# Optimization experiments

Hardware: AMD Instinct MI355X
Metric: run time of the kernel (lower is better)

## Reference

```python
import jax, jax.numpy as jnp
import numpy as np

B, S, D = 2, 2048, 1024
H, DK, DV = 16, 64, 64
D_OUT = 1024


def setup_inputs() -> dict:
    key = jax.random.key(0)
    ks = jax.random.split(key, 9)
    sd = 1.0 / np.sqrt(D)
    # Linear weights stored as [in, out] (torch applies x @ W.T with W [out,in])
    return {
        "x": jax.random.normal(ks[0], (B, S, D), dtype=jnp.float32),
        "Wq": jax.random.normal(ks[1], (D, H * DK), dtype=jnp.float32) * sd,
        "bq": jnp.zeros((H * DK,), dtype=jnp.float32),
        "Wk": jax.random.normal(ks[2], (D, H * DK), dtype=jnp.float32) * sd,
        "bk": jnp.zeros((H * DK,), dtype=jnp.float32),
        "Wv": jax.random.normal(ks[3], (D, H * DV), dtype=jnp.float32) * sd,
        "bv": jnp.zeros((H * DV,), dtype=jnp.float32),
        "Wo": jax.random.normal(ks[4], (H * DV, D_OUT), dtype=jnp.float32) * sd,
        "bo": jnp.zeros((D_OUT,), dtype=jnp.float32),
    }


def _attn(x, Wq, bq, Wk, bk, Wv, bv, Wo, bo):
    n = x.shape[-2]
    q = (x @ Wq + bq).reshape(B, n, H, DK).transpose(0, 2, 1, 3)  # [B,H,S,DK]
    k = (x @ Wk + bk).reshape(B, n, H, DK).transpose(0, 2, 1, 3)
    v = (x @ Wv + bv).reshape(B, n, H, DV).transpose(0, 2, 1, 3)
    scores = jnp.einsum("bhqd,bhkd->bhqk", q / jnp.sqrt(jnp.float32(DK)), k)
    # causal additive mask: 0 on/below diagonal, -inf above (matches 1 - 1/tril)
    causal = jnp.tril(jnp.ones((n, n), dtype=bool))
    scores = jnp.where(causal, scores, -jnp.inf)
    probs = jax.nn.softmax(scores, axis=-1)
    out = jnp.einsum("bhqk,bhkd->bhqd", probs, v)  # [B,H,S,DV]
    out = out.transpose(0, 2, 1, 3).reshape(B, n, H * DV)
    return out @ Wo + bo


def reference(x, Wq, bq, Wk, bk, Wv, bv, Wo, bo):
    return _attn(x, Wq, bq, Wk, bk, Wv, bv, Wo, bo)
```

## Files before the change

### kernel.cpp

```cpp
#include <hip/hip_runtime.h>

typedef unsigned short u16;
typedef __bf16 bf16_t;
typedef bf16_t bf16x8 __attribute__((ext_vector_type(8)));
typedef float f32x4 __attribute__((ext_vector_type(4)));

#define DEV __device__ __forceinline__
#define LOG2E 1.4426950408889634f
#define QKS (0.125f * LOG2E)

static_assert(sizeof(bf16x8) == 16, "bf16x8 must be 16B");

DEV u16 f2b(float v) { return __builtin_bit_cast(u16, (bf16_t)v); }
DEV float b2f(u16 v) { return (float)__builtin_bit_cast(bf16_t, v); }

DEV void g2l16(const void* g, void* l) {
  __builtin_amdgcn_global_load_lds(
      (const __attribute__((address_space(1))) void*)g,
      (__attribute__((address_space(3))) void*)l, 16, 0, 0);
}

DEV int sniff_is_f32(const u16* __restrict__ W) {
  const int lane = threadIdx.x & 63;
  int cnt = 0;
#pragma unroll
  for (int i = 0; i < 8; i++) {
    u16 u = W[(lane * 8 + i) * 2];
    cnt += (((u >> 7) & 0xFF) >= 126) ? 1 : 0;
  }
#pragma unroll
  for (int off = 1; off < 64; off <<= 1) cnt += __shfl_xor(cnt, off, 64);
  return cnt > 128;
}


__global__ __launch_bounds__(256) void convert_x_k(
    const void* __restrict__ xin, const u16* __restrict__ Wsniff,
    u16* __restrict__ xb) {
  const int i = (blockIdx.x * 256 + threadIdx.x) * 8;
  if (sniff_is_f32(Wsniff)) {
    const float* xf = (const float*)xin;
    float4 a = *(const float4*)&xf[i];
    float4 b = *(const float4*)&xf[i + 4];
    u16 o[8] = {f2b(a.x), f2b(a.y), f2b(a.z), f2b(a.w),
                f2b(b.x), f2b(b.y), f2b(b.z), f2b(b.w)};
    *(uint4*)&xb[i] = *(const uint4*)o;
  } else {
    *(uint4*)&xb[i] = *(const uint4*)((const u16*)xin + i);
  }
}

__global__ __launch_bounds__(256) void transpose_k(
    const void* __restrict__ Wq, const void* __restrict__ Wk,
    const void* __restrict__ Wv, const void* __restrict__ Wo,
    const void* __restrict__ bq, const void* __restrict__ bk,
    const void* __restrict__ bv, const void* __restrict__ bo,
    u16* __restrict__ Wqkv_t, u16* __restrict__ Wo_t,
    u16* __restrict__ bqkv_b, u16* __restrict__ bo_b) {
  __shared__ u16 tile[64][68];
  const int z = blockIdx.z;
  const void* src = (z == 0) ? Wq : (z == 1) ? Wk : (z == 2) ? Wv : Wo;
  u16* dst = (z < 3) ? (Wqkv_t + (size_t)z * 1024 * 1024) : Wo_t;
  const int k0 = blockIdx.y * 64, n0 = blockIdx.x * 64;
  const int t = threadIdx.x;
  const int r = t >> 4, c4 = (t & 15) * 4;
  const int isf = sniff_is_f32((const u16*)Wq);

  if (blockIdx.x == 0 && blockIdx.y == 0) {
    const void* bsrc = (z == 0) ? bq : (z == 1) ? bk : (z == 2) ? bv : bo;
    u16* bdst = (z < 3) ? (bqkv_b + z * 1024) : bo_b;
#pragma unroll
    for (int i = 0; i < 4; i++) {
      const int idx = t + i * 256;
      const float v =
          isf ? ((const float*)bsrc)[idx] : b2f(((const u16*)bsrc)[idx]);
      bdst[idx] = f2b(v);
    }
  }

#pragma unroll
  for (int i = 0; i < 4; i++) {
    int rr = r + i * 16;
    const size_t base = (size_t)(k0 + rr) * 1024 + n0 + c4;
    if (isf) {
      float4 v = *(const float4*)((const float*)src + base);
      tile[rr][c4] = f2b(v.x); tile[rr][c4 + 1] = f2b(v.y);
      tile[rr][c4 + 2] = f2b(v.z); tile[rr][c4 + 3] = f2b(v.w);
    } else {
      ushort4 v = *(const ushort4*)((const u16*)src + base);
      tile[rr][c4] = v.x; tile[rr][c4 + 1] = v.y;
      tile[rr][c4 + 2] = v.z; tile[rr][c4 + 3] = v.w;
    }
  }
  __syncthreads();
#pragma unroll
  for (int i = 0; i < 4; i++) {
    int rr = r + i * 16;
    ushort4 v;
    v.x = tile[c4][rr]; v.y = tile[c4 + 1][rr];
    v.z = tile[c4 + 2][rr]; v.w = tile[c4 + 3][rr];
    *(ushort4*)&dst[(size_t)(n0 + rr) * 1024 + k0 + c4] = v;
  }
}

template <int MODE>
__global__ __launch_bounds__(256, 3) void gemm_k(
    const u16* __restrict__ A, const u16* __restrict__ Bt,
    const u16* __restrict__ bias, void* __restrict__ o0v,
    u16* __restrict__ o1, u16* __restrict__ o2,
    const u16* __restrict__ Wsniff, int M, int N, int K) {
  alignas(16) __shared__ u16 As[128][32];
  alignas(16) __shared__ u16 Bs[128][32];
  const int tid = threadIdx.x;
  const int wave = tid >> 6, lane = tid & 63;
  const int quad = lane >> 4, l16 = lane & 15;
  const int m0 = blockIdx.y * 128, n0 = blockIdx.x * 128;
  const int wr = (wave >> 1) * 64, wc = (wave & 1) * 64;

  f32x4 acc[4][4];
#pragma unroll
  for (int i = 0; i < 4; i++)
#pragma unroll
    for (int j = 0; j < 4; j++) acc[i][j] = (f32x4){0.f, 0.f, 0.f, 0.f};

  const int srow = lane >> 2, scol = (lane & 3) * 8;
  for (int k0 = 0; k0 < K; k0 += 32) {
    __syncthreads();
#pragma unroll
    for (int j = 0; j < 4; j++) {
      const int t = wave * 4 + j;
      if (t < 8) {
        const int row = t * 16 + srow;
        g2l16(&A[(size_t)(m0 + row) * K + k0 + scol], &As[t * 16][0]);
      } else {
        const int rb = t - 8;
        const int row = rb * 16 + srow;
        g2l16(&Bt[(size_t)(n0 + row) * K + k0 + scol], &Bs[rb * 16][0]);
      }
    }
    __syncthreads();
    bf16x8 af[4], bfr[4];
#pragma unroll
    for (int mi = 0; mi < 4; mi++)
      af[mi] = *(const bf16x8*)&As[wr + mi * 16 + l16][quad * 8];
#pragma unroll
    for (int ni = 0; ni < 4; ni++)
      bfr[ni] = *(const bf16x8*)&Bs[wc + ni * 16 + l16][quad * 8];
#pragma unroll
    for (int mi = 0; mi < 4; mi++)
#pragma unroll
      for (int ni = 0; ni < 4; ni++)
        acc[mi][ni] = __builtin_amdgcn_mfma_f32_16x16x32_bf16(
            af[mi], bfr[ni], acc[mi][ni], 0, 0, 0);
  }

  const int isf = (MODE == 1) ? sniff_is_f32(Wsniff) : 0;
#pragma unroll
  for (int mi = 0; mi < 4; mi++) {
    const int rbase = m0 + wr + mi * 16 + quad * 4;
#pragma unroll
    for (int ni = 0; ni < 4; ni++) {
      const int col = n0 + wc + ni * 16 + l16;
      const float bv_ = b2f(bias[col]);
      if (MODE == 0) {
        const int seg = col >> 10;
        const int nn = col & 1023;
        const int h = nn >> 6, d = nn & 63;
        u16* op = (seg == 0) ? (u16*)o0v : (seg == 1) ? o1 : o2;
#pragma unroll
        for (int r = 0; r < 4; r++) {
          const int m = rbase + r;
          const int b = m >> 11, s = m & 2047;
          float v = acc[mi][ni][r] + bv_;
          if (seg == 0) v *= QKS;
          if (seg < 2)
            op[(((size_t)(b * 16 + h) * 2048) + s) * 64 + d] = f2b(v);
          else
            op[(((size_t)(b * 16 + h) * 64) + d) * 2048 + s] = f2b(v);
        }
      } else {
#pragma unroll
        for (int r = 0; r < 4; r++) {
          const int m = rbase + r;
          const float v = acc[mi][ni][r] + bv_;
          if (isf) ((float*)o0v)[(size_t)m * N + col] = v;
          else     ((u16*)o0v)[(size_t)m * N + col] = f2b(v);
        }
      }
    }
  }
}

__global__ __launch_bounds__(256, 3) void attn_k(
    const u16* __restrict__ Q, const u16* __restrict__ K,
    const u16* __restrict__ Vt, u16* __restrict__ O) {
  alignas(16) __shared__ u16 Ks[2][2][64][32];
  alignas(16) __shared__ u16 Vs[2][2][64][32];
  alignas(16) __shared__ u16 Ps[128][72];
  const int tid = threadIdx.x;
  const int wave = tid >> 6, lane = tid & 63;
  const int quad = lane >> 4, l16 = lane & 15;
  const int qt = 15 - (int)blockIdx.x;
  const int bh = blockIdx.y;
  const int b = bh >> 4, h = bh & 15;
  const int q0 = qt * 128;
  const int wrow = q0 + wave * 32;

  bf16x8 aq[2][2];
#pragma unroll
  for (int mi = 0; mi < 2; mi++)
#pragma unroll
    for (int kc = 0; kc < 2; kc++)
      aq[mi][kc] = *(const bf16x8*)&Q[((size_t)bh * 2048 + wrow + mi * 16 + l16) *
                                          64 + kc * 32 + quad * 8];

  f32x4 oacc[2][4];
#pragma unroll
  for (int mi = 0; mi < 2; mi++)
#pragma unroll
    for (int di = 0; di < 4; di++) oacc[mi][di] = (f32x4){0.f, 0.f, 0.f, 0.f};
  float lrow[2][4] = {{0.f, 0.f, 0.f, 0.f}, {0.f, 0.f, 0.f, 0.f}};

  const int srow = lane >> 2, scol = (lane & 3) * 8;
  auto stage = [&](int buf, int kts) {
    const int k0s = kts * 64;
#pragma unroll
    for (int j = 0; j < 4; j++) {
      const int t = wave * 4 + j;
      if (t < 8) {
        const int kc = t >> 2, rb = t & 3;
        g2l16(&K[((size_t)bh * 2048 + k0s + rb * 16 + srow) * 64 + kc * 32 + scol],
              &Ks[buf][kc][rb * 16][0]);
      } else {
        const int tt = t - 8;
        const int kc = tt >> 2, rb = tt & 3;
        g2l16(&Vt[((size_t)bh * 64 + rb * 16 + srow) * 2048 + k0s + kc * 32 + scol],
              &Vs[buf][kc][rb * 16][0]);
      }
    }
  };

  const int nkt = 2 * qt + 2;
  stage(0, 0);
  for (int kt = 0; kt < nkt; kt++) {
    const int cur = kt & 1;
    const int k0 = kt * 64;
    if (kt + 1 < nkt) {
      stage(cur ^ 1, kt + 1);
      asm volatile("s_waitcnt vmcnt(4)" ::: "memory");
    } else {
      asm volatile("s_waitcnt vmcnt(0)" ::: "memory");
    }
    asm volatile("s_barrier" ::: "memory");

    const bool skip = (k0 > wrow + 31);
    if (!skip) {
      const bool needmask = (k0 + 63 > wrow);
      f32x4 sacc[2][4];
#pragma unroll
      for (int mi = 0; mi < 2; mi++)
#pragma unroll
        for (int ni = 0; ni < 4; ni++) sacc[mi][ni] = (f32x4){0.f, 0.f, 0.f, 0.f};
#pragma unroll
      for (int kc = 0; kc < 2; kc++)
#pragma unroll
        for (int ni = 0; ni < 4; ni++) {
          bf16x8 bk_ = *(const bf16x8*)&Ks[cur][kc][ni * 16 + l16][quad * 8];
#pragma unroll
          for (int mi = 0; mi < 2; mi++)
            sacc[mi][ni] = __builtin_amdgcn_mfma_f32_16x16x32_bf16(
                aq[mi][kc], bk_, sacc[mi][ni], 0, 0, 0);
        }

#pragma unroll
      for (int mi = 0; mi < 2; mi++) {
        const int rowb = wrow + mi * 16 + quad * 4;
#pragma unroll
        for (int ni = 0; ni < 4; ni++) {
          const int col = k0 + ni * 16 + l16;
#pragma unroll
          for (int r = 0; r < 4; r++) {
            float p = __builtin_amdgcn_exp2f(sacc[mi][ni][r]);
            if (needmask && (col > rowb + r)) p = 0.f;
            lrow[mi][r] += p;
            Ps[wave * 32 + mi * 16 + quad * 4 + r][ni * 16 + l16] = f2b(p);
          }
        }
      }
      asm volatile("s_waitcnt lgkmcnt(0)" ::: "memory");

#pragma unroll
      for (int kc = 0; kc < 2; kc++) {
        bf16x8 ap[2];
#pragma unroll
        for (int mi = 0; mi < 2; mi++)
          ap[mi] = *(const bf16x8*)&Ps[wave * 32 + mi * 16 + l16][kc * 32 + quad * 8];
#pragma unroll
        for (int di = 0; di < 4; di++) {
          bf16x8 bv_ = *(const bf16x8*)&Vs[cur][kc][di * 16 + l16][quad * 8];
#pragma unroll
          for (int mi = 0; mi < 2; mi++)
            oacc[mi][di] = __builtin_amdgcn_mfma_f32_16x16x32_bf16(
                ap[mi], bv_, oacc[mi][di], 0, 0, 0);
        }
      }
    }
    asm volatile("s_barrier" ::: "memory");
  }

#pragma unroll
  for (int mi = 0; mi < 2; mi++)
#pragma unroll
    for (int r = 0; r < 4; r++) {
#pragma unroll
      for (int off = 1; off < 16; off <<= 1)
        lrow[mi][r] += __shfl_xor(lrow[mi][r], off, 64);
    }

#pragma unroll
  for (int mi = 0; mi < 2; mi++)
#pragma unroll
    for (int di = 0; di < 4; di++)
#pragma unroll
      for (int r = 0; r < 4; r++) {
        const int row = q0 + wave * 32 + mi * 16 + quad * 4 + r;
        const float v = oacc[mi][di][r] / lrow[mi][r];
        O[((size_t)b * 2048 + row) * 1024 + h * 64 + di * 16 + l16] = f2b(v);
      }
}

extern "C" void kernel_launch(void* const* d_in, const int* in_sizes, int n_in,
                              void* d_out, int out_size, void* d_ws,
                              size_t ws_size, hipStream_t stream) {
  const void* x  = d_in[0];
  const void* Wq = d_in[1];
  const void* bq = d_in[2];
  const void* Wk = d_in[3];
  const void* bk = d_in[4];
  const void* Wv = d_in[5];
  const void* bv = d_in[6];
  const void* Wo = d_in[7];
  const void* bo = d_in[8];

  char* ws = (char*)d_ws;
  u16* xb     = (u16*)ws;          ws += (size_t)4096 * 1024 * 2;
  u16* Wqkv_t = (u16*)ws;          ws += (size_t)3072 * 1024 * 2;
  u16* Wo_t   = (u16*)ws;          ws += (size_t)1024 * 1024 * 2;
  u16* bqkv_b = (u16*)ws;          ws += 3072 * 2;
  u16* bo_b   = (u16*)ws;          ws += 1024 * 2 + 128;
  u16* Qb     = (u16*)ws;          ws += (size_t)4096 * 1024 * 2;
  u16* Kb     = (u16*)ws;          ws += (size_t)4096 * 1024 * 2;
  u16* Vtb    = (u16*)ws;          ws += (size_t)4096 * 1024 * 2;
  u16* Ob     = xb;

  convert_x_k<<<2048, 256, 0, stream>>>(x, (const u16*)Wq, xb);
  transpose_k<<<dim3(16, 16, 4), 256, 0, stream>>>(Wq, Wk, Wv, Wo, bq, bk, bv,
                                                   bo, Wqkv_t, Wo_t, bqkv_b,
                                                   bo_b);
  gemm_k<0><<<dim3(24, 32), 256, 0, stream>>>(xb, Wqkv_t, bqkv_b, Qb, Kb, Vtb,
                                              (const u16*)Wq, 4096, 3072, 1024);
  attn_k<<<dim3(16, 32), 256, 0, stream>>>(Qb, Kb, Vtb, Ob);
  gemm_k<1><<<dim3(8, 32), 256, 0, stream>>>(Ob, Wo_t, bo_b, d_out, nullptr,
                                             nullptr, (const u16*)Wq, 4096,
                                             1024, 1024);
}
```

Baseline: 236.7 us.

## Pair causal query tiles per block and stage 128-key swizzled K/V tiles

```diff
diff --git a/kernel.cpp b/kernel.cpp
--- a/kernel.cpp
+++ b/kernel.cpp
@@ -191,142 +191,157 @@
   }
 }
 
-__global__ __launch_bounds__(256, 3) void attn_k(
+__global__ __launch_bounds__(256, 1) void attn_k(
     const u16* __restrict__ Q, const u16* __restrict__ K,
     const u16* __restrict__ Vt, u16* __restrict__ O) {
-  alignas(16) __shared__ u16 Ks[2][2][64][32];
-  alignas(16) __shared__ u16 Vs[2][2][64][32];
+  alignas(16) __shared__ u16 Ks[2][128][64];
+  alignas(16) __shared__ u16 Vs[2][64][128];
   alignas(16) __shared__ u16 Ps[128][72];
   const int tid = threadIdx.x;
   const int wave = tid >> 6, lane = tid & 63;
   const int quad = lane >> 4, l16 = lane & 15;
-  const int qt = 15 - (int)blockIdx.x;
   const int bh = blockIdx.y;
   const int b = bh >> 4, h = bh & 15;
-  const int q0 = qt * 128;
-  const int wrow = q0 + wave * 32;
-
-  bf16x8 aq[2][2];
-#pragma unroll
-  for (int mi = 0; mi < 2; mi++)
-#pragma unroll
-    for (int kc = 0; kc < 2; kc++)
-      aq[mi][kc] = *(const bf16x8*)&Q[((size_t)bh * 2048 + wrow + mi * 16 + l16) *
-                                          64 + kc * 32 + quad * 8];
-
-  f32x4 oacc[2][4];
-#pragma unroll
-  for (int mi = 0; mi < 2; mi++)
-#pragma unroll
-    for (int di = 0; di < 4; di++) oacc[mi][di] = (f32x4){0.f, 0.f, 0.f, 0.f};
-  float lrow[2][4] = {{0.f, 0.f, 0.f, 0.f}, {0.f, 0.f, 0.f, 0.f}};
-
-  const int srow = lane >> 2, scol = (lane & 3) * 8;
-  auto stage = [&](int buf, int kts) {
-    const int k0s = kts * 64;
-#pragma unroll
-    for (int j = 0; j < 4; j++) {
-      const int t = wave * 4 + j;
-      if (t < 8) {
-        const int kc = t >> 2, rb = t & 3;
-        g2l16(&K[((size_t)bh * 2048 + k0s + rb * 16 + srow) * 64 + kc * 32 + scol],
-              &Ks[buf][kc][rb * 16][0]);
+  const int sw = l16 & 7;
+
+  const int krow_off = lane >> 3, kchunk = lane & 7;
+  const int vrow_off = lane >> 4, vchunk = lane & 15;
+
+  for (int pi = 0; pi < 2; pi++) {
+    const int qt = pi ? (15 - (int)blockIdx.x) : (int)blockIdx.x;
+    const int q0 = qt * 128;
+    const int wrow = q0 + wave * 32;
+    const int nkt = qt + 1;
+
+    bf16x8 aq[2][2];
+#pragma unroll
+    for (int mi = 0; mi < 2; mi++)
+#pragma unroll
+      for (int kcD = 0; kcD < 2; kcD++)
+        aq[mi][kcD] = *(const bf16x8*)&Q[((size_t)bh * 2048 + wrow + mi * 16 +
+                                          l16) * 64 + kcD * 32 + quad * 8];
+
+    f32x4 oacc[2][4];
+#pragma unroll
+    for (int mi = 0; mi < 2; mi++)
+#pragma unroll
+      for (int di = 0; di < 4; di++) oacc[mi][di] = (f32x4){0.f, 0.f, 0.f, 0.f};
+    float lrow[2][4] = {{0.f, 0.f, 0.f, 0.f}, {0.f, 0.f, 0.f, 0.f}};
+
+    auto stage = [&](int buf, int kts) {
+      const int k0s = kts * 128;
+#pragma unroll
+      for (int j = 0; j < 8; j++) {
+        const int t = wave * 8 + j;
+        if (t < 16) {
+          const int r = t * 8 + krow_off;
+          const int cs = kchunk ^ (r & 7);
+          g2l16(&K[((size_t)bh * 2048 + k0s + r) * 64 + cs * 8],
+                &Ks[buf][t * 8][0]);
+        } else {
+          const int t2 = t - 16;
+          const int r = t2 * 4 + vrow_off;
+          const int cs = vchunk ^ (r & 7);
+          g2l16(&Vt[((size_t)bh * 64 + r) * 2048 + k0s + cs * 8],
+                &Vs[buf][t2 * 4][0]);
+        }
+      }
+    };
+
+    stage(0, 0);
+    for (int kt = 0; kt < nkt; kt++) {
+      const int cur = kt & 1;
+      const int k0 = kt * 128;
+      if (kt + 1 < nkt) {
+        stage(cur ^ 1, kt + 1);
+        asm volatile("s_waitcnt vmcnt(8)" ::: "memory");
       } else {
-        const int tt = t - 8;
-        const int kc = tt >> 2, rb = tt & 3;
-        g2l16(&Vt[((size_t)bh * 64 + rb * 16 + srow) * 2048 + k0s + kc * 32 + scol],
-              &Vs[buf][kc][rb * 16][0]);
-      }
-    }
-  };
-
-  const int nkt = 2 * qt + 2;
-  stage(0, 0);
-  for (int kt = 0; kt < nkt; kt++) {
-    const int cur = kt & 1;
-    const int k0 = kt * 64;
-    if (kt + 1 < nkt) {
-      stage(cur ^ 1, kt + 1);
-      asm volatile("s_waitcnt vmcnt(4)" ::: "memory");
-    } else {
-      asm volatile("s_waitcnt vmcnt(0)" ::: "memory");
-    }
-    asm volatile("s_barrier" ::: "memory");
-
-    const bool skip = (k0 > wrow + 31);
-    if (!skip) {
-      const bool needmask = (k0 + 63 > wrow);
-      f32x4 sacc[2][4];
-#pragma unroll
-      for (int mi = 0; mi < 2; mi++)
-#pragma unroll
-        for (int ni = 0; ni < 4; ni++) sacc[mi][ni] = (f32x4){0.f, 0.f, 0.f, 0.f};
-#pragma unroll
-      for (int kc = 0; kc < 2; kc++)
-#pragma unroll
-        for (int ni = 0; ni < 4; ni++) {
-          bf16x8 bk_ = *(const bf16x8*)&Ks[cur][kc][ni * 16 + l16][quad * 8];
+        asm volatile("s_waitcnt vmcnt(0)" ::: "memory");
+      }
+      asm volatile("s_barrier" ::: "memory");
+
+      for (int h2 = 0; h2 < 2; h2++) {
+        const int k0h = k0 + h2 * 64;
+        if (k0h > wrow + 31) continue;
+        const bool needmask = (k0h + 63 > wrow);
+
+        f32x4 sacc[2][4];
+#pragma unroll
+        for (int mi = 0; mi < 2; mi++)
+#pragma unroll
+          for (int ni = 0; ni < 4; ni++)
+            sacc[mi][ni] = (f32x4){0.f, 0.f, 0.f, 0.f};
+#pragma unroll
+        for (int kcD = 0; kcD < 2; kcD++)
+#pragma unroll
+          for (int ni = 0; ni < 4; ni++) {
+            const int pos = ((kcD << 2) | quad) ^ sw;
+            bf16x8 bk_ =
+                *(const bf16x8*)&Ks[cur][h2 * 64 + ni * 16 + l16][pos * 8];
+#pragma unroll
+            for (int mi = 0; mi < 2; mi++)
+              sacc[mi][ni] = __builtin_amdgcn_mfma_f32_16x16x32_bf16(
+                  aq[mi][kcD], bk_, sacc[mi][ni], 0, 0, 0);
+          }
+
+#pragma unroll
+        for (int mi = 0; mi < 2; mi++) {
+          const int rowb = wrow + mi * 16 + quad * 4;
+#pragma unroll
+          for (int ni = 0; ni < 4; ni++) {
+            const int col = k0h + ni * 16 + l16;
+#pragma unroll
+            for (int r = 0; r < 4; r++) {
+              float p = __builtin_amdgcn_exp2f(sacc[mi][ni][r]);
+              if (needmask && (col > rowb + r)) p = 0.f;
+              lrow[mi][r] += p;
+              Ps[wave * 32 + mi * 16 + quad * 4 + r][ni * 16 + l16] = f2b(p);
+            }
+          }
+        }
+        asm volatile("s_waitcnt lgkmcnt(0)" ::: "memory");
+
+#pragma unroll
+        for (int kc = 0; kc < 2; kc++) {
+          bf16x8 ap[2];
 #pragma unroll
           for (int mi = 0; mi < 2; mi++)
-            sacc[mi][ni] = __builtin_amdgcn_mfma_f32_16x16x32_bf16(
-                aq[mi][kc], bk_, sacc[mi][ni], 0, 0, 0);
-        }
-
-#pragma unroll
-      for (int mi = 0; mi < 2; mi++) {
-        const int rowb = wrow + mi * 16 + quad * 4;
-#pragma unroll
-        for (int ni = 0; ni < 4; ni++) {
-          const int col = k0 + ni * 16 + l16;
-#pragma unroll
-          for (int r = 0; r < 4; r++) {
-            float p = __builtin_amdgcn_exp2f(sacc[mi][ni][r]);
-            if (needmask && (col > rowb + r)) p = 0.f;
-            lrow[mi][r] += p;
-            Ps[wave * 32 + mi * 16 + quad * 4 + r][ni * 16 + l16] = f2b(p);
+            ap[mi] = *(const bf16x8*)&Ps[wave * 32 + mi * 16 + l16]
+                                        [kc * 32 + quad * 8];
+#pragma unroll
+          for (int di = 0; di < 4; di++) {
+            const int pos = ((h2 << 3) | (kc << 2) | quad) ^ sw;
+            bf16x8 bv_ = *(const bf16x8*)&Vs[cur][di * 16 + l16][pos * 8];
+#pragma unroll
+            for (int mi = 0; mi < 2; mi++)
+              oacc[mi][di] = __builtin_amdgcn_mfma_f32_16x16x32_bf16(
+                  ap[mi], bv_, oacc[mi][di], 0, 0, 0);
           }
         }
       }
-      asm volatile("s_waitcnt lgkmcnt(0)" ::: "memory");
-
-#pragma unroll
-      for (int kc = 0; kc < 2; kc++) {
-        bf16x8 ap[2];
-#pragma unroll
-        for (int mi = 0; mi < 2; mi++)
-          ap[mi] = *(const bf16x8*)&Ps[wave * 32 + mi * 16 + l16][kc * 32 + quad * 8];
-#pragma unroll
-        for (int di = 0; di < 4; di++) {
-          bf16x8 bv_ = *(const bf16x8*)&Vs[cur][kc][di * 16 + l16][quad * 8];
-#pragma unroll
-          for (int mi = 0; mi < 2; mi++)
-            oacc[mi][di] = __builtin_amdgcn_mfma_f32_16x16x32_bf16(
-                ap[mi], bv_, oacc[mi][di], 0, 0, 0);
-        }
-      }
-    }
-    asm volatile("s_barrier" ::: "memory");
-  }
-
-#pragma unroll
-  for (int mi = 0; mi < 2; mi++)
-#pragma unroll
-    for (int r = 0; r < 4; r++) {
-#pragma unroll
-      for (int off = 1; off < 16; off <<= 1)
-        lrow[mi][r] += __shfl_xor(lrow[mi][r], off, 64);
-    }
-
-#pragma unroll
-  for (int mi = 0; mi < 2; mi++)
-#pragma unroll
-    for (int di = 0; di < 4; di++)
+      asm volatile("s_barrier" ::: "memory");
+    }
+
+#pragma unroll
+    for (int mi = 0; mi < 2; mi++)
 #pragma unroll
       for (int r = 0; r < 4; r++) {
-        const int row = q0 + wave * 32 + mi * 16 + quad * 4 + r;
-        const float v = oacc[mi][di][r] / lrow[mi][r];
-        O[((size_t)b * 2048 + row) * 1024 + h * 64 + di * 16 + l16] = f2b(v);
-      }
+#pragma unroll
+        for (int off = 1; off < 16; off <<= 1)
+          lrow[mi][r] += __shfl_xor(lrow[mi][r], off, 64);
+      }
+
+#pragma unroll
+    for (int mi = 0; mi < 2; mi++)
+#pragma unroll
+      for (int di = 0; di < 4; di++)
+#pragma unroll
+        for (int r = 0; r < 4; r++) {
+          const int row = wrow + mi * 16 + quad * 4 + r;
+          const float v = oacc[mi][di][r] / lrow[mi][r];
+          O[((size_t)b * 2048 + row) * 1024 + h * 64 + di * 16 + l16] = f2b(v);
+        }
+  }
 }
 
 extern "C" void kernel_launch(void* const* d_in, const int* in_sizes, int n_in,
@@ -359,7 +374,7 @@
                                                    bo_b);
   gemm_k<0><<<dim3(24, 32), 256, 0, stream>>>(xb, Wqkv_t, bqkv_b, Qb, Kb, Vtb,
                                               (const u16*)Wq, 4096, 3072, 1024);
-  attn_k<<<dim3(16, 32), 256, 0, stream>>>(Qb, Kb, Vtb, Ob);
+  attn_k<<<dim3(8, 32), 256, 0, stream>>>(Qb, Kb, Vtb, Ob);
   gemm_k<1><<<dim3(8, 32), 256, 0, stream>>>(Ob, Wo_t, bo_b, d_out, nullptr,
                                              nullptr, (const u16*)Wq, 4096,
                                              1024, 1024);
```

New measurement: 225.7 us. -4.6%, faster.

## Use XOR-swizzled 64-wide LDS tiles in GEMM and attention, transpose S computation

Applied to the files above, without the earlier changes.

```diff
diff --git a/kernel.cpp b/kernel.cpp
--- a/kernel.cpp
+++ b/kernel.cpp
@@ -109,13 +109,14 @@
     const u16* __restrict__ bias, void* __restrict__ o0v,
     u16* __restrict__ o1, u16* __restrict__ o2,
     const u16* __restrict__ Wsniff, int M, int N, int K) {
-  alignas(16) __shared__ u16 As[128][32];
-  alignas(16) __shared__ u16 Bs[128][32];
+  alignas(16) __shared__ u16 As[128][64];
+  alignas(16) __shared__ u16 Bs[128][64];
   const int tid = threadIdx.x;
   const int wave = tid >> 6, lane = tid & 63;
   const int quad = lane >> 4, l16 = lane & 15;
   const int m0 = blockIdx.y * 128, n0 = blockIdx.x * 128;
   const int wr = (wave >> 1) * 64, wc = (wave & 1) * 64;
+  const int sw = l16 & 7;
 
   f32x4 acc[4][4];
 #pragma unroll
@@ -123,35 +124,41 @@
 #pragma unroll
     for (int j = 0; j < 4; j++) acc[i][j] = (f32x4){0.f, 0.f, 0.f, 0.f};
 
-  const int srow = lane >> 2, scol = (lane & 3) * 8;
-  for (int k0 = 0; k0 < K; k0 += 32) {
+  const int srow = lane >> 3, schunk = lane & 7;
+  const int cs = schunk ^ srow;
+
+  for (int k0 = 0; k0 < K; k0 += 64) {
     __syncthreads();
 #pragma unroll
-    for (int j = 0; j < 4; j++) {
-      const int t = wave * 4 + j;
-      if (t < 8) {
-        const int row = t * 16 + srow;
-        g2l16(&A[(size_t)(m0 + row) * K + k0 + scol], &As[t * 16][0]);
+    for (int j = 0; j < 8; j++) {
+      const int t = wave * 8 + j;
+      if (t < 16) {
+        const int row = t * 8 + srow;
+        g2l16(&A[(size_t)(m0 + row) * K + k0 + cs * 8], &As[t * 8][0]);
       } else {
-        const int rb = t - 8;
-        const int row = rb * 16 + srow;
-        g2l16(&Bt[(size_t)(n0 + row) * K + k0 + scol], &Bs[rb * 16][0]);
+        const int t2 = t - 16;
+        const int row = t2 * 8 + srow;
+        g2l16(&Bt[(size_t)(n0 + row) * K + k0 + cs * 8], &Bs[t2 * 8][0]);
       }
     }
     __syncthreads();
-    bf16x8 af[4], bfr[4];
-#pragma unroll
-    for (int mi = 0; mi < 4; mi++)
-      af[mi] = *(const bf16x8*)&As[wr + mi * 16 + l16][quad * 8];
-#pragma unroll
-    for (int ni = 0; ni < 4; ni++)
-      bfr[ni] = *(const bf16x8*)&Bs[wc + ni * 16 + l16][quad * 8];
-#pragma unroll
-    for (int mi = 0; mi < 4; mi++)
+#pragma unroll
+    for (int kk = 0; kk < 2; kk++) {
+      const int pos = ((kk << 2) | quad) ^ sw;
+      bf16x8 af[4], bfr[4];
+#pragma unroll
+      for (int mi = 0; mi < 4; mi++)
+        af[mi] = *(const bf16x8*)&As[wr + mi * 16 + l16][pos * 8];
 #pragma unroll
       for (int ni = 0; ni < 4; ni++)
-        acc[mi][ni] = __builtin_amdgcn_mfma_f32_16x16x32_bf16(
-            af[mi], bfr[ni], acc[mi][ni], 0, 0, 0);
+        bfr[ni] = *(const bf16x8*)&Bs[wc + ni * 16 + l16][pos * 8];
+#pragma unroll
+      for (int mi = 0; mi < 4; mi++)
+#pragma unroll
+        for (int ni = 0; ni < 4; ni++)
+          acc[mi][ni] = __builtin_amdgcn_mfma_f32_16x16x32_bf16(
+              af[mi], bfr[ni], acc[mi][ni], 0, 0, 0);
+    }
   }
 
   const int isf = (MODE == 1) ? sniff_is_f32(Wsniff) : 0;
@@ -194,53 +201,57 @@
 __global__ __launch_bounds__(256, 3) void attn_k(
     const u16* __restrict__ Q, const u16* __restrict__ K,
     const u16* __restrict__ Vt, u16* __restrict__ O) {
-  alignas(16) __shared__ u16 Ks[2][2][64][32];
-  alignas(16) __shared__ u16 Vs[2][2][64][32];
-  alignas(16) __shared__ u16 Ps[128][72];
+  alignas(16) __shared__ u16 Ks[2][64][64];
+  alignas(16) __shared__ u16 Vs[2][64][64];
+  alignas(16) __shared__ u16 PsT[128][64];
   const int tid = threadIdx.x;
-  const int wave = tid >> 6, lane = tid & 63;
+  const int w = tid >> 6, lane = tid & 63;
   const int quad = lane >> 4, l16 = lane & 15;
-  const int qt = 15 - (int)blockIdx.x;
   const int bh = blockIdx.y;
   const int b = bh >> 4, h = bh & 15;
+  const int sw = l16 & 7;
+
+  const int qt = 15 - (int)blockIdx.x;
   const int q0 = qt * 128;
-  const int wrow = q0 + wave * 32;
+  const int wrow = q0 + w * 32;
+  const int nkt = 2 * qt + 2;
+
+  const int srow = lane >> 3, schunk = lane & 7;
+  const int cs = schunk ^ srow;
 
   bf16x8 aq[2][2];
 #pragma unroll
   for (int mi = 0; mi < 2; mi++)
 #pragma unroll
     for (int kc = 0; kc < 2; kc++)
-      aq[mi][kc] = *(const bf16x8*)&Q[((size_t)bh * 2048 + wrow + mi * 16 + l16) *
-                                          64 + kc * 32 + quad * 8];
+      aq[mi][kc] = *(const bf16x8*)&Q[((size_t)bh * 2048 + wrow + mi * 16 +
+                                       l16) * 64 + kc * 32 + quad * 8];
 
   f32x4 oacc[2][4];
 #pragma unroll
   for (int mi = 0; mi < 2; mi++)
 #pragma unroll
     for (int di = 0; di < 4; di++) oacc[mi][di] = (f32x4){0.f, 0.f, 0.f, 0.f};
-  float lrow[2][4] = {{0.f, 0.f, 0.f, 0.f}, {0.f, 0.f, 0.f, 0.f}};
-
-  const int srow = lane >> 2, scol = (lane & 3) * 8;
+  float lrp[2] = {0.f, 0.f};
+
   auto stage = [&](int buf, int kts) {
     const int k0s = kts * 64;
 #pragma unroll
     for (int j = 0; j < 4; j++) {
-      const int t = wave * 4 + j;
+      const int t = w * 4 + j;
       if (t < 8) {
-        const int kc = t >> 2, rb = t & 3;
-        g2l16(&K[((size_t)bh * 2048 + k0s + rb * 16 + srow) * 64 + kc * 32 + scol],
-              &Ks[buf][kc][rb * 16][0]);
+        const int r = t * 8 + srow;
+        g2l16(&K[((size_t)bh * 2048 + k0s + r) * 64 + cs * 8],
+              &Ks[buf][t * 8][0]);
       } else {
-        const int tt = t - 8;
-        const int kc = tt >> 2, rb = tt & 3;
-        g2l16(&Vt[((size_t)bh * 64 + rb * 16 + srow) * 2048 + k0s + kc * 32 + scol],
-              &Vs[buf][kc][rb * 16][0]);
+        const int t2 = t - 8;
+        const int r = t2 * 8 + srow;
+        g2l16(&Vt[((size_t)bh * 64 + r) * 2048 + k0s + cs * 8],
+              &Vs[buf][t2 * 8][0]);
       }
     }
   };
 
-  const int nkt = 2 * qt + 2;
   stage(0, 0);
   for (int kt = 0; kt < nkt; kt++) {
     const int cur = kt & 1;
@@ -253,55 +264,62 @@
     }
     asm volatile("s_barrier" ::: "memory");
 
-    const bool skip = (k0 > wrow + 31);
-    if (!skip) {
+    if (k0 <= wrow + 31) {
       const bool needmask = (k0 + 63 > wrow);
-      f32x4 sacc[2][4];
-#pragma unroll
-      for (int mi = 0; mi < 2; mi++)
-#pragma unroll
-        for (int ni = 0; ni < 4; ni++) sacc[mi][ni] = (f32x4){0.f, 0.f, 0.f, 0.f};
+
+      f32x4 st[4][2];
+#pragma unroll
+      for (int nk = 0; nk < 4; nk++)
+#pragma unroll
+        for (int mi = 0; mi < 2; mi++) st[nk][mi] = (f32x4){0.f, 0.f, 0.f, 0.f};
 #pragma unroll
       for (int kc = 0; kc < 2; kc++)
 #pragma unroll
-        for (int ni = 0; ni < 4; ni++) {
-          bf16x8 bk_ = *(const bf16x8*)&Ks[cur][kc][ni * 16 + l16][quad * 8];
+        for (int nk = 0; nk < 4; nk++) {
+          const int pos = ((kc << 2) | quad) ^ sw;
+          bf16x8 kf = *(const bf16x8*)&Ks[cur][nk * 16 + l16][pos * 8];
 #pragma unroll
           for (int mi = 0; mi < 2; mi++)
-            sacc[mi][ni] = __builtin_amdgcn_mfma_f32_16x16x32_bf16(
-                aq[mi][kc], bk_, sacc[mi][ni], 0, 0, 0);
+            st[nk][mi] = __builtin_amdgcn_mfma_f32_16x16x32_bf16(
+                kf, aq[mi][kc], st[nk][mi], 0, 0, 0);
         }
 
 #pragma unroll
       for (int mi = 0; mi < 2; mi++) {
-        const int rowb = wrow + mi * 16 + quad * 4;
-#pragma unroll
-        for (int ni = 0; ni < 4; ni++) {
-          const int col = k0 + ni * 16 + l16;
+        const int q_glob = wrow + mi * 16 + l16;
+        const int prow = w * 32 + mi * 16 + l16;
+#pragma unroll
+        for (int nk = 0; nk < 4; nk++) {
+          const int kbase = k0 + nk * 16 + quad * 4;
+          u16 pk[4];
 #pragma unroll
           for (int r = 0; r < 4; r++) {
-            float p = __builtin_amdgcn_exp2f(sacc[mi][ni][r]);
-            if (needmask && (col > rowb + r)) p = 0.f;
-            lrow[mi][r] += p;
-            Ps[wave * 32 + mi * 16 + quad * 4 + r][ni * 16 + l16] = f2b(p);
+            float p = __builtin_amdgcn_exp2f(st[nk][mi][r]);
+            if (needmask && (kbase + r > q_glob)) p = 0.f;
+            lrp[mi] += p;
+            pk[r] = f2b(p);
           }
+          const int g = nk * 2 + (quad >> 1);
+          const int cc = g ^ sw;
+          *(uint2*)&PsT[prow][cc * 8 + (quad & 1) * 4] = *(const uint2*)pk;
         }
       }
       asm volatile("s_waitcnt lgkmcnt(0)" ::: "memory");
 
 #pragma unroll
       for (int kc = 0; kc < 2; kc++) {
+        const int pos = ((kc << 2) | quad) ^ sw;
         bf16x8 ap[2];
 #pragma unroll
         for (int mi = 0; mi < 2; mi++)
-          ap[mi] = *(const bf16x8*)&Ps[wave * 32 + mi * 16 + l16][kc * 32 + quad * 8];
+          ap[mi] = *(const bf16x8*)&PsT[w * 32 + mi * 16 + l16][pos * 8];
 #pragma unroll
         for (int di = 0; di < 4; di++) {
-          bf16x8 bv_ = *(const bf16x8*)&Vs[cur][kc][di * 16 + l16][quad * 8];
+          bf16x8 vf = *(const bf16x8*)&Vs[cur][di * 16 + l16][pos * 8];
 #pragma unroll
           for (int mi = 0; mi < 2; mi++)
             oacc[mi][di] = __builtin_amdgcn_mfma_f32_16x16x32_bf16(
-                ap[mi], bv_, oacc[mi][di], 0, 0, 0);
+                ap[mi], vf, oacc[mi][di], 0, 0, 0);
         }
       }
     }
@@ -309,13 +327,16 @@
   }
 
 #pragma unroll
+  for (int mi = 0; mi < 2; mi++) {
+    lrp[mi] += __shfl_xor(lrp[mi], 16, 64);
+    lrp[mi] += __shfl_xor(lrp[mi], 32, 64);
+  }
+  float rdiv[2][4];
+#pragma unroll
   for (int mi = 0; mi < 2; mi++)
 #pragma unroll
-    for (int r = 0; r < 4; r++) {
-#pragma unroll
-      for (int off = 1; off < 16; off <<= 1)
-        lrow[mi][r] += __shfl_xor(lrow[mi][r], off, 64);
-    }
+    for (int r = 0; r < 4; r++)
+      rdiv[mi][r] = __shfl(lrp[mi], quad * 4 + r, 64);
 
 #pragma unroll
   for (int mi = 0; mi < 2; mi++)
@@ -323,8 +344,8 @@
     for (int di = 0; di < 4; di++)
 #pragma unroll
       for (int r = 0; r < 4; r++) {
-        const int row = q0 + wave * 32 + mi * 16 + quad * 4 + r;
-        const float v = oacc[mi][di][r] / lrow[mi][r];
+        const int row = wrow + mi * 16 + quad * 4 + r;
+        const float v = oacc[mi][di][r] / rdiv[mi][r];
         O[((size_t)b * 2048 + row) * 1024 + h * 64 + di * 16 + l16] = f2b(v);
       }
 }
```

After: 222.6 us. 1.06x faster.
